# Optimization experiments

Measured on AMD Instinct MI355X. Metric: run time of the kernel, lower is better.

Reference implementation:

```python
import jax, jax.numpy as jnp
import numpy as np


def setup_inputs() -> dict:
    key = jax.random.key(0)
    ks = jax.random.split(key, 4)
    B, T, D, U = 256, 4096, 3, 8
    d = D + 1                      # time-augmented path dimension
    sig_dim = 1 + d + d * d        # depth-2 signature incl. constant term = 21
    glorot = jax.nn.initializers.glorot_uniform()
    return {
        "inputs": jax.random.normal(ks[0], (B, T, D), jnp.float32),
        "input_kernel": glorot(ks[1], (D, 3 * U), jnp.float32),
        "recurrent_kernel": glorot(ks[2], (U, 3 * U), jnp.float32),
        "forget_kernel": glorot(ks[3], (sig_dim, U), jnp.float32),
        "bias": jnp.zeros((4 * U,), jnp.float32),
    }


def _streamed_signature_depth2(path):
    """Streamed (cumulative) truncated signature of depth 2 via Chen's identity.
    path: (B, T, d) -> (B, T, 1 + d + d*d). Entry t is the signature of path[:t+1]."""
    B, T, d = path.shape
    dx = jnp.diff(path, axis=1)                                   # (B, T-1, d)
    L1 = jnp.cumsum(dx, axis=1)                                   # level-1
    L1_prev = jnp.concatenate([jnp.zeros((B, 1, d), path.dtype), L1[:, :-1]], axis=1)
    # Chen: L2_t = L2_{t-1} + L1_{t-1} (x) dx_t + 0.5 dx_t (x) dx_t
    terms = L1_prev[..., :, None] * dx[..., None, :] + 0.5 * dx[..., :, None] * dx[..., None, :]
    L2 = jnp.cumsum(terms, axis=1).reshape(B, T - 1, d * d)       # level-2
    sig = jnp.concatenate([jnp.ones((B, T - 1, 1), path.dtype), L1, L2], axis=-1)
    sig0 = jnp.concatenate(
        [jnp.ones((B, 1, 1), path.dtype), jnp.zeros((B, 1, d + d * d), path.dtype)], axis=-1)
    return jnp.concatenate([sig0, sig], axis=1)                   # (B, T, sig_dim)


def reference(inputs, input_kernel, recurrent_kernel, forget_kernel, bias):
    B, T, D = inputs.shape
    U = recurrent_kernel.shape[0]
    t_grid = jnp.linspace(0.0, 1.0, T)
    path = jnp.concatenate(
        [jnp.broadcast_to(t_grid[None, :, None], (B, T, 1)), inputs], axis=-1)
    sig = _streamed_signature_depth2(path)                        # (B, T, sig_dim)
    # normalize signatures at times t>0 by elapsed time (as in the original)
    sig = sig.at[:, 1:, :].set(sig[:, 1:, :] / t_grid[1:, None])

    b_i, b_f, b_c, b_o = jnp.split(bias, 4)
    x_proj = jnp.einsum('btd,du->btu', inputs, input_kernel)      # (B, T, 3U)

    def step(carry, xs):
        h, c = carry
        x_t, sig_t = xs
        gates = h @ recurrent_kernel + x_t                        # (B, 3U)
        i_t, c_hat, o_t = jnp.split(gates, 3, axis=-1)
        f_t = jax.nn.sigmoid(sig_t @ forget_kernel + b_f)         # signature forget gate
        i_t = jax.nn.sigmoid(i_t + b_i)
        c_hat = jnp.tanh(c_hat + b_c)
        o_t = jax.nn.sigmoid(o_t + b_o)
        c_new = f_t * c + i_t * c_hat
        h_new = o_t * jnp.tanh(c_new)
        return (h_new, c_new), h_new

    h0 = jnp.zeros((B, U), inputs.dtype)
    (_, _), h_seq = jax.lax.scan(
        step, (h0, h0), (x_proj.transpose(1, 0, 2), sig.transpose(1, 0, 2)))
    return h_seq.transpose(1, 0, 2)                               # (B, T, U)
```

## Files before the change

### kernel.cpp

```cpp
#include <hip/hip_runtime.h>
#include <hip/hip_bf16.h>

#define TT 4096
#define BB 256
#define DD 3
#define UU 8

#if defined(__has_builtin)
#if __has_builtin(__builtin_amdgcn_exp2f) && __has_builtin(__builtin_amdgcn_rcpf)
#define FAST_EXP2(x) __builtin_amdgcn_exp2f(x)
#define FAST_RCP(x)  __builtin_amdgcn_rcpf(x)
#endif
#endif
#ifndef FAST_EXP2
#define FAST_EXP2(x) exp2f(x)
#define FAST_RCP(x)  (1.0f / (x))
#endif

__device__ __forceinline__ float fsig(float x) {
    float e = FAST_EXP2(-1.4426950408889634f * x);
    return FAST_RCP(1.0f + e);
}
__device__ __forceinline__ float ftanh(float x) {
    float e = FAST_EXP2(2.8853900817779268f * x);
    return 1.0f - 2.0f * FAST_RCP(1.0f + e);
}

template <int CTRL>
__device__ __forceinline__ float dpp_f(float v) {
    int i = __builtin_bit_cast(int, v);
    i = __builtin_amdgcn_update_dpp(0, i, CTRL, 0xF, 0xF, true);
    return __builtin_bit_cast(float, i);
}

__device__ __forceinline__ float block_excl_scan(float v, int tid, float* red) {
    float x = v;
    int lid = tid & 63;
    #pragma unroll
    for (int d = 1; d < 64; d <<= 1) {
        float y = __shfl_up(x, d, 64);
        if (lid >= d) x += y;
    }
    int wave = tid >> 6;
    __syncthreads();
    if (lid == 63) red[wave] = x;
    __syncthreads();
    float off = 0.0f;
    for (int w = 0; w < wave; ++w) off += red[w];
    return off + (x - v);
}

__global__ __launch_bounds__(256) void sig_pre_kernel(
    const float* __restrict__ x,
    const float* __restrict__ Wi,
    const float* __restrict__ Wf,
    const float* __restrict__ bias,
    float* __restrict__ ws)
{
    __shared__ float sWf[21 * 8];
    __shared__ float sWi[3 * 24];
    __shared__ float sB[32];
    __shared__ float red[4];

    const int tid = threadIdx.x;
    const int b = blockIdx.x;
    if (tid < 168) sWf[tid] = Wf[tid];
    if (tid < 72)  sWi[tid] = Wi[tid];
    if (tid < 32)  sB[tid]  = bias[tid];
    __syncthreads();

    const float dtc = 1.0f / 4095.0f;
    const int t0 = tid * 16;
    const float* xb = x + (size_t)b * TT * DD;

    float l1[4] = {0.f, 0.f, 0.f, 0.f};
    float l2[16];
    #pragma unroll
    for (int i = 0; i < 16; ++i) l2[i] = 0.f;
    {
        int s = (tid == 0) ? 1 : t0;
        float xp0 = xb[(s - 1) * 3 + 0];
        float xp1 = xb[(s - 1) * 3 + 1];
        float xp2 = xb[(s - 1) * 3 + 2];
        for (; s < t0 + 16; ++s) {
            float c0 = xb[s * 3 + 0], c1 = xb[s * 3 + 1], c2 = xb[s * 3 + 2];
            float dxv[4] = {dtc, c0 - xp0, c1 - xp1, c2 - xp2};
            #pragma unroll
            for (int r = 0; r < 4; ++r) {
                float tr = l1[r] + 0.5f * dxv[r];
                #pragma unroll
                for (int cc = 0; cc < 4; ++cc)
                    l2[r * 4 + cc] = fmaf(tr, dxv[cc], l2[r * 4 + cc]);
            }
            #pragma unroll
            for (int r = 0; r < 4; ++r) l1[r] += dxv[r];
            xp0 = c0; xp1 = c1; xp2 = c2;
        }
    }

    float S1[4], O1[4];
    #pragma unroll
    for (int r = 0; r < 4; ++r) { S1[r] = l1[r]; }
    for (int r = 0; r < 4; ++r) O1[r] = block_excl_scan(S1[r], tid, red);
    float O2[16];
    for (int rc = 0; rc < 16; ++rc) {
        float c2v = l2[rc] + O1[rc >> 2] * S1[rc & 3];
        O2[rc] = block_excl_scan(c2v, tid, red);
    }

    #pragma unroll
    for (int r = 0; r < 4; ++r) l1[r] = O1[r];
    #pragma unroll
    for (int i = 0; i < 16; ++i) l2[i] = O2[i];

    float xp0, xp1, xp2;
    {
        int tp = (tid == 0) ? 0 : (t0 - 1);
        xp0 = xb[tp * 3 + 0]; xp1 = xb[tp * 3 + 1]; xp2 = xb[tp * 3 + 2];
    }
    for (int i2 = 0; i2 < 16; ++i2) {
        const int t = t0 + i2;
        float c0 = xb[t * 3 + 0], c1 = xb[t * 3 + 1], c2 = xb[t * 3 + 2];
        if (t > 0) {
            float dxv[4] = {dtc, c0 - xp0, c1 - xp1, c2 - xp2};
            #pragma unroll
            for (int r = 0; r < 4; ++r) {
                float tr = l1[r] + 0.5f * dxv[r];
                #pragma unroll
                for (int cc = 0; cc < 4; ++cc)
                    l2[r * 4 + cc] = fmaf(tr, dxv[cc], l2[r * 4 + cc]);
            }
            #pragma unroll
            for (int r = 0; r < 4; ++r) l1[r] += dxv[r];
        }
        xp0 = c0; xp1 = c1; xp2 = c2;
        const float scale = (t == 0) ? 1.0f : (4095.0f / (float)t);
        float sg[21];
        sg[0] = scale;
        #pragma unroll
        for (int r = 0; r < 4; ++r) sg[1 + r] = l1[r] * scale;
        #pragma unroll
        for (int rc = 0; rc < 16; ++rc) sg[5 + rc] = l2[rc] * scale;

        float fa[8];
        #pragma unroll
        for (int u = 0; u < 8; ++u) fa[u] = sB[8 + u];
        #pragma unroll
        for (int j = 0; j < 21; ++j) {
            float s = sg[j];
            #pragma unroll
            for (int u = 0; u < 8; ++u) fa[u] = fmaf(s, sWf[j * 8 + u], fa[u]);
        }
        float g[24];
        #pragma unroll
        for (int u = 0; u < 8; ++u) {
            g[u] = sB[u]; g[8 + u] = sB[16 + u]; g[16 + u] = sB[24 + u];
        }
        #pragma unroll
        for (int gg = 0; gg < 24; ++gg) {
            g[gg] = fmaf(c0, sWi[gg], g[gg]);
            g[gg] = fmaf(c1, sWi[24 + gg], g[gg]);
            g[gg] = fmaf(c2, sWi[48 + gg], g[gg]);
        }
        float4* wp = (float4*)ws + ((size_t)t * BB + b) * UU;
        #pragma unroll
        for (int u = 0; u < 8; ++u)
            wp[u] = make_float4(g[u], g[8 + u], g[16 + u], fsig(fa[u]));
    }
}

__global__ __launch_bounds__(64) void lstm_scan_full(
    const float* __restrict__ ws, const float* __restrict__ Wr,
    float* __restrict__ out)
{
    const int lane = threadIdx.x;
    const int u = lane & 7;
    const int b = blockIdx.x * 8 + (lane >> 3);
    float wa[8], wb[8], wc[8];
    #pragma unroll
    for (int m = 0; m < 8; ++m) {
        int j = u ^ m;
        wa[m] = Wr[j * 24 + u];
        wb[m] = Wr[j * 24 + 8 + u];
        wc[m] = Wr[j * 24 + 16 + u];
    }
    const float4* gp = (const float4*)ws + (size_t)b * 8 + u;
    float4 buf[8];
    #pragma unroll
    for (int p = 0; p < 8; ++p) buf[p] = gp[(size_t)p * 2048];
    float h = 0.f, c = 0.f;
    float* op = out + (size_t)b * TT * 8 + u;

    auto step = [&](int t, float4 g) {
        float h1 = dpp_f<0xB1>(h);
        float h2 = dpp_f<0x4E>(h);
        float h3 = dpp_f<0x1B>(h);
        float h7 = dpp_f<0x141>(h);
        float h6 = dpp_f<0xB1>(h7);
        float h5 = dpp_f<0x4E>(h7);
        float h4 = dpp_f<0x1B>(h7);
        float gi = fmaf(h, wa[0], g.x), giB = h4 * wa[4];
        float gc = fmaf(h, wb[0], g.y), gcB = h4 * wb[4];
        float go = fmaf(h, wc[0], g.z), goB = h4 * wc[4];
        gi = fmaf(h1, wa[1], gi);  giB = fmaf(h5, wa[5], giB);
        gc = fmaf(h1, wb[1], gc);  gcB = fmaf(h5, wb[5], gcB);
        go = fmaf(h1, wc[1], go);  goB = fmaf(h5, wc[5], goB);
        gi = fmaf(h2, wa[2], gi);  giB = fmaf(h6, wa[6], giB);
        gc = fmaf(h2, wb[2], gc);  gcB = fmaf(h6, wb[6], gcB);
        go = fmaf(h2, wc[2], go);  goB = fmaf(h6, wc[6], goB);
        gi = fmaf(h3, wa[3], gi);  giB = fmaf(h7, wa[7], giB);
        gc = fmaf(h3, wb[3], gc);  gcB = fmaf(h7, wb[7], gcB);
        go = fmaf(h3, wc[3], go);  goB = fmaf(h7, wc[7], goB);
        gi += giB; gc += gcB; go += goB;
        float iv = fsig(gi);
        float cv = ftanh(gc);
        float ov = fsig(go);
        c = fmaf(g.w, c, iv * cv);
        h = ov * ftanh(c);
        op[(size_t)t * 8] = h;
    };

    for (int tb = 0; tb + 8 < TT; tb += 8) {
        #pragma unroll
        for (int j = 0; j < 8; ++j) {
            const int t = tb + j;
            float4 g = buf[j];
            buf[j] = gp[(size_t)(t + 8) * 2048];
            step(t, g);
        }
    }
    #pragma unroll
    for (int j = 0; j < 8; ++j) step(TT - 8 + j, buf[j]);
}

__global__ __launch_bounds__(64) void lstm_scan_ultra(
    const float* __restrict__ x, const float* __restrict__ Wi,
    const float* __restrict__ Wr, const float* __restrict__ Wf,
    const float* __restrict__ bias, float* __restrict__ out)
{
    const int lane = threadIdx.x;
    const int u = lane & 7;
    const int q = lane >> 3;
    const int b = blockIdx.x * 8 + q;
    float wa[8], wb[8], wc[8];
    #pragma unroll
    for (int m = 0; m < 8; ++m) {
        int j = u ^ m;
        wa[m] = Wr[j * 24 + u];
        wb[m] = Wr[j * 24 + 8 + u];
        wc[m] = Wr[j * 24 + 16 + u];
    }
    float wia[3], wib[3], wic[3];
    #pragma unroll
    for (int k = 0; k < 3; ++k) {
        wia[k] = Wi[k * 24 + u];
        wib[k] = Wi[k * 24 + 8 + u];
        wic[k] = Wi[k * 24 + 16 + u];
    }
    float wf[21];
    #pragma unroll
    for (int j = 0; j < 21; ++j) wf[j] = Wf[j * 8 + u];
    const float bi = bias[u], bf = bias[8 + u], bc = bias[16 + u], bo = bias[24 + u];
    const float* xb = x + (size_t)b * TT * 3;
    float l1[4] = {0.f, 0.f, 0.f, 0.f};
    float l2[16];
    #pragma unroll
    for (int i = 0; i < 16; ++i) l2[i] = 0.f;
    float xp0 = xb[0], xp1 = xb[1], xp2 = xb[2];
    float h = 0.f, c = 0.f;
    float* op = out + (size_t)b * TT * 8 + u;
    const float dtc = 1.0f / 4095.0f;
    for (int t = 0; t < TT; ++t) {
        float c0 = xb[t * 3 + 0], c1 = xb[t * 3 + 1], c2 = xb[t * 3 + 2];
        if (t > 0) {
            float dxv[4] = {dtc, c0 - xp0, c1 - xp1, c2 - xp2};
            #pragma unroll
            for (int r = 0; r < 4; ++r) {
                float tr = l1[r] + 0.5f * dxv[r];
                #pragma unroll
                for (int cc = 0; cc < 4; ++cc)
                    l2[r * 4 + cc] = fmaf(tr, dxv[cc], l2[r * 4 + cc]);
            }
            #pragma unroll
            for (int r = 0; r < 4; ++r) l1[r] += dxv[r];
        }
        xp0 = c0; xp1 = c1; xp2 = c2;
        const float scale = (t == 0) ? 1.0f : (4095.0f / (float)t);
        float dot = wf[0];
        #pragma unroll
        for (int r = 0; r < 4; ++r) dot = fmaf(l1[r], wf[1 + r], dot);
        #pragma unroll
        for (int rc = 0; rc < 16; ++rc) dot = fmaf(l2[rc], wf[5 + rc], dot);
        float fv = fsig(fmaf(scale, dot, bf));
        float gi = bi, gc = bc, go = bo;
        gi = fmaf(c0, wia[0], gi); gi = fmaf(c1, wia[1], gi); gi = fmaf(c2, wia[2], gi);
        gc = fmaf(c0, wib[0], gc); gc = fmaf(c1, wib[1], gc); gc = fmaf(c2, wib[2], gc);
        go = fmaf(c0, wic[0], go); go = fmaf(c1, wic[1], go); go = fmaf(c2, wic[2], go);
        float h1 = dpp_f<0xB1>(h);
        float h2 = dpp_f<0x4E>(h);
        float h3 = dpp_f<0x1B>(h);
        float h7 = dpp_f<0x141>(h);
        float h6 = dpp_f<0xB1>(h7);
        float h5 = dpp_f<0x4E>(h7);
        float h4 = dpp_f<0x1B>(h7);
        gi = fmaf(h, wa[0], gi); gi = fmaf(h1, wa[1], gi); gi = fmaf(h2, wa[2], gi); gi = fmaf(h3, wa[3], gi);
        gi = fmaf(h4, wa[4], gi); gi = fmaf(h5, wa[5], gi); gi = fmaf(h6, wa[6], gi); gi = fmaf(h7, wa[7], gi);
        gc = fmaf(h, wb[0], gc); gc = fmaf(h1, wb[1], gc); gc = fmaf(h2, wb[2], gc); gc = fmaf(h3, wb[3], gc);
        gc = fmaf(h4, wb[4], gc); gc = fmaf(h5, wb[5], gc); gc = fmaf(h6, wb[6], gc); gc = fmaf(h7, wb[7], gc);
        go = fmaf(h, wc[0], go); go = fmaf(h1, wc[1], go); go = fmaf(h2, wc[2], go); go = fmaf(h3, wc[3], go);
        go = fmaf(h4, wc[4], go); go = fmaf(h5, wc[5], go); go = fmaf(h6, wc[6], go); go = fmaf(h7, wc[7], go);
        float iv = fsig(gi);
        float cv = ftanh(gc);
        float ov = fsig(go);
        c = fmaf(fv, c, iv * cv);
        h = ov * ftanh(c);
        op[(size_t)t * 8] = h;
    }
}

extern "C" void kernel_launch(void* const* d_in, const int* in_sizes, int n_in,
                              void* d_out, int out_size, void* d_ws, size_t ws_size,
                              hipStream_t stream) {
    const float* x    = (const float*)d_in[0];
    const float* Wi   = (const float*)d_in[1];
    const float* Wr   = (const float*)d_in[2];
    const float* Wf   = (const float*)d_in[3];
    const float* bias = (const float*)d_in[4];
    float* out = (float*)d_out;

    const size_t need = (size_t)TT * BB * UU * 4 * sizeof(float);
    if (ws_size >= need) {
        sig_pre_kernel<<<dim3(BB), dim3(256), 0, stream>>>(x, Wi, Wf, bias, (float*)d_ws);
        lstm_scan_full<<<dim3(BB / 8), dim3(64), 0, stream>>>((const float*)d_ws, Wr, out);
    } else {
        lstm_scan_ultra<<<dim3(BB / 8), dim3(64), 0, stream>>>(x, Wi, Wr, Wf, bias, out);
    }
}
```

Measured before the change: 652.5 us.

## Fold log2e scaling into weights, merge gate reciprocals, use DPP wave scans

Pre-scales the input, recurrent, forget weights and biases by -log2e or 2log2e so the activation exponents need no extra multiply. In the recurrent step, each pair of sigmoid/tanh reciprocals is combined into a single reciprocal of a product, which shortens the per-step serial dependency chain. The signature precompute now loads its inputs as vectorised registers, replaces the shuffle-based block scans with DPP wave scans plus one shared-memory pass, and applies the time normalisation once after the forget-gate dot product. The trade-off is slightly different rounding behaviour and a clamp needed to avoid overflow in the merged expressions.

```diff
diff --git a/kernel.cpp b/kernel.cpp
--- a/kernel.cpp
+++ b/kernel.cpp
@@ -17,13 +17,12 @@
 #define FAST_RCP(x)  (1.0f / (x))
 #endif
 
+#define NLOG2E  (-1.4426950408889634f)
+#define P2LOG2E ( 2.8853900817779268f)
+
 __device__ __forceinline__ float fsig(float x) {
-    float e = FAST_EXP2(-1.4426950408889634f * x);
+    float e = FAST_EXP2(NLOG2E * x);
     return FAST_RCP(1.0f + e);
-}
-__device__ __forceinline__ float ftanh(float x) {
-    float e = FAST_EXP2(2.8853900817779268f * x);
-    return 1.0f - 2.0f * FAST_RCP(1.0f + e);
 }
 
 template <int CTRL>
@@ -32,22 +31,19 @@
     i = __builtin_amdgcn_update_dpp(0, i, CTRL, 0xF, 0xF, true);
     return __builtin_bit_cast(float, i);
 }
-
-__device__ __forceinline__ float block_excl_scan(float v, int tid, float* red) {
-    float x = v;
-    int lid = tid & 63;
-    #pragma unroll
-    for (int d = 1; d < 64; d <<= 1) {
-        float y = __shfl_up(x, d, 64);
-        if (lid >= d) x += y;
-    }
-    int wave = tid >> 6;
-    __syncthreads();
-    if (lid == 63) red[wave] = x;
-    __syncthreads();
-    float off = 0.0f;
-    for (int w = 0; w < wave; ++w) off += red[w];
-    return off + (x - v);
+template <int CTRL, int RM>
+__device__ __forceinline__ float dpp_add(float x) {
+    int t = __builtin_amdgcn_update_dpp(0, __builtin_bit_cast(int, x), CTRL, RM, 0xF, true);
+    return x + __builtin_bit_cast(float, t);
+}
+__device__ __forceinline__ float wave_incl_scan(float v) {
+    v = dpp_add<0x111, 0xF>(v);
+    v = dpp_add<0x112, 0xF>(v);
+    v = dpp_add<0x114, 0xF>(v);
+    v = dpp_add<0x118, 0xF>(v);
+    v = dpp_add<0x142, 0xA>(v);
+    v = dpp_add<0x143, 0xC>(v);
+    return v;
 }
 
 __global__ __launch_bounds__(256) void sig_pre_kernel(
@@ -57,34 +53,57 @@
     const float* __restrict__ bias,
     float* __restrict__ ws)
 {
-    __shared__ float sWf[21 * 8];
-    __shared__ float sWi[3 * 24];
+    __shared__ float sWf[168];
+    __shared__ float sWi[72];
     __shared__ float sB[32];
-    __shared__ float red[4];
+    __shared__ float tot1[4 * 4];
+    __shared__ float tot2[4 * 16];
 
     const int tid = threadIdx.x;
     const int b = blockIdx.x;
-    if (tid < 168) sWf[tid] = Wf[tid];
-    if (tid < 72)  sWi[tid] = Wi[tid];
-    if (tid < 32)  sB[tid]  = bias[tid];
+    if (tid < 168) sWf[tid] = NLOG2E * Wf[tid];
+    if (tid < 72) {
+        int col = tid % 24;
+        float s = (col < 8) ? NLOG2E : (col < 16) ? P2LOG2E : NLOG2E;
+        sWi[tid] = s * Wi[tid];
+    }
+    if (tid < 32) {
+        float s = (tid < 16) ? NLOG2E : (tid < 24) ? P2LOG2E : NLOG2E;
+        sB[tid] = s * bias[tid];
+    }
     __syncthreads();
 
     const float dtc = 1.0f / 4095.0f;
     const int t0 = tid * 16;
+    const int lid = tid & 63;
+    const int wv = tid >> 6;
     const float* xb = x + (size_t)b * TT * DD;
+
+    float xs[48];
+    {
+        const float4* xv = (const float4*)(xb + (size_t)t0 * 3);
+        #pragma unroll
+        for (int k = 0; k < 12; ++k) {
+            float4 v = xv[k];
+            xs[k * 4 + 0] = v.x; xs[k * 4 + 1] = v.y;
+            xs[k * 4 + 2] = v.z; xs[k * 4 + 3] = v.w;
+        }
+    }
+    float pp0, pp1, pp2;
+    if (tid == 0) { pp0 = xs[0]; pp1 = xs[1]; pp2 = xs[2]; }
+    else { pp0 = xb[t0 * 3 - 3]; pp1 = xb[t0 * 3 - 2]; pp2 = xb[t0 * 3 - 1]; }
 
     float l1[4] = {0.f, 0.f, 0.f, 0.f};
     float l2[16];
     #pragma unroll
     for (int i = 0; i < 16; ++i) l2[i] = 0.f;
     {
-        int s = (tid == 0) ? 1 : t0;
-        float xp0 = xb[(s - 1) * 3 + 0];
-        float xp1 = xb[(s - 1) * 3 + 1];
-        float xp2 = xb[(s - 1) * 3 + 2];
-        for (; s < t0 + 16; ++s) {
-            float c0 = xb[s * 3 + 0], c1 = xb[s * 3 + 1], c2 = xb[s * 3 + 2];
-            float dxv[4] = {dtc, c0 - xp0, c1 - xp1, c2 - xp2};
+        float xp0 = pp0, xp1 = pp1, xp2 = pp2;
+        #pragma unroll
+        for (int i = 0; i < 16; ++i) {
+            float c0 = xs[i * 3], c1 = xs[i * 3 + 1], c2 = xs[i * 3 + 2];
+            float d0 = (tid == 0 && i == 0) ? 0.f : dtc;
+            float dxv[4] = {d0, c0 - xp0, c1 - xp1, c2 - xp2};
             #pragma unroll
             for (int r = 0; r < 4; ++r) {
                 float tr = l1[r] + 0.5f * dxv[r];
@@ -98,14 +117,34 @@
         }
     }
 
-    float S1[4], O1[4];
-    #pragma unroll
-    for (int r = 0; r < 4; ++r) { S1[r] = l1[r]; }
-    for (int r = 0; r < 4; ++r) O1[r] = block_excl_scan(S1[r], tid, red);
-    float O2[16];
+    float I1[4], O1[4];
+    #pragma unroll
+    for (int r = 0; r < 4; ++r) {
+        I1[r] = wave_incl_scan(l1[r]);
+        if (lid == 63) tot1[wv * 4 + r] = I1[r];
+    }
+    __syncthreads();
+    #pragma unroll
+    for (int r = 0; r < 4; ++r) {
+        float off = 0.f;
+        for (int w = 0; w < wv; ++w) off += tot1[w * 4 + r];
+        O1[r] = off + I1[r] - l1[r];
+    }
+
+    float I2[16], cin[16], O2[16];
+    #pragma unroll
     for (int rc = 0; rc < 16; ++rc) {
-        float c2v = l2[rc] + O1[rc >> 2] * S1[rc & 3];
-        O2[rc] = block_excl_scan(c2v, tid, red);
+        float c2v = l2[rc] + O1[rc >> 2] * l1[rc & 3];
+        cin[rc] = c2v;
+        I2[rc] = wave_incl_scan(c2v);
+        if (lid == 63) tot2[wv * 16 + rc] = I2[rc];
+    }
+    __syncthreads();
+    #pragma unroll
+    for (int rc = 0; rc < 16; ++rc) {
+        float off = 0.f;
+        for (int w = 0; w < wv; ++w) off += tot2[w * 16 + rc];
+        O2[rc] = off + I2[rc] - cin[rc];
     }
 
     #pragma unroll
@@ -113,43 +152,39 @@
     #pragma unroll
     for (int i = 0; i < 16; ++i) l2[i] = O2[i];
 
-    float xp0, xp1, xp2;
-    {
-        int tp = (tid == 0) ? 0 : (t0 - 1);
-        xp0 = xb[tp * 3 + 0]; xp1 = xb[tp * 3 + 1]; xp2 = xb[tp * 3 + 2];
-    }
+    float xp0 = pp0, xp1 = pp1, xp2 = pp2;
+    #pragma unroll
     for (int i2 = 0; i2 < 16; ++i2) {
         const int t = t0 + i2;
-        float c0 = xb[t * 3 + 0], c1 = xb[t * 3 + 1], c2 = xb[t * 3 + 2];
-        if (t > 0) {
-            float dxv[4] = {dtc, c0 - xp0, c1 - xp1, c2 - xp2};
-            #pragma unroll
-            for (int r = 0; r < 4; ++r) {
-                float tr = l1[r] + 0.5f * dxv[r];
-                #pragma unroll
-                for (int cc = 0; cc < 4; ++cc)
-                    l2[r * 4 + cc] = fmaf(tr, dxv[cc], l2[r * 4 + cc]);
-            }
-            #pragma unroll
-            for (int r = 0; r < 4; ++r) l1[r] += dxv[r];
-        }
+        float c0 = xs[i2 * 3], c1 = xs[i2 * 3 + 1], c2 = xs[i2 * 3 + 2];
+        float d0 = (tid == 0 && i2 == 0) ? 0.f : dtc;
+        float dxv[4] = {d0, c0 - xp0, c1 - xp1, c2 - xp2};
+        #pragma unroll
+        for (int r = 0; r < 4; ++r) {
+            float tr = l1[r] + 0.5f * dxv[r];
+            #pragma unroll
+            for (int cc = 0; cc < 4; ++cc)
+                l2[r * 4 + cc] = fmaf(tr, dxv[cc], l2[r * 4 + cc]);
+        }
+        #pragma unroll
+        for (int r = 0; r < 4; ++r) l1[r] += dxv[r];
         xp0 = c0; xp1 = c1; xp2 = c2;
+
         const float scale = (t == 0) ? 1.0f : (4095.0f / (float)t);
-        float sg[21];
-        sg[0] = scale;
-        #pragma unroll
-        for (int r = 0; r < 4; ++r) sg[1 + r] = l1[r] * scale;
-        #pragma unroll
-        for (int rc = 0; rc < 16; ++rc) sg[5 + rc] = l2[rc] * scale;
-
         float fa[8];
         #pragma unroll
-        for (int u = 0; u < 8; ++u) fa[u] = sB[8 + u];
-        #pragma unroll
-        for (int j = 0; j < 21; ++j) {
-            float s = sg[j];
-            #pragma unroll
-            for (int u = 0; u < 8; ++u) fa[u] = fmaf(s, sWf[j * 8 + u], fa[u]);
+        for (int u = 0; u < 8; ++u) fa[u] = sWf[u];
+        #pragma unroll
+        for (int r = 0; r < 4; ++r) {
+            float s = l1[r];
+            #pragma unroll
+            for (int u = 0; u < 8; ++u) fa[u] = fmaf(s, sWf[(1 + r) * 8 + u], fa[u]);
+        }
+        #pragma unroll
+        for (int rc = 0; rc < 16; ++rc) {
+            float s = l2[rc];
+            #pragma unroll
+            for (int u = 0; u < 8; ++u) fa[u] = fmaf(s, sWf[(5 + rc) * 8 + u], fa[u]);
         }
         float g[24];
         #pragma unroll
@@ -164,8 +199,11 @@
         }
         float4* wp = (float4*)ws + ((size_t)t * BB + b) * UU;
         #pragma unroll
-        for (int u = 0; u < 8; ++u)
-            wp[u] = make_float4(g[u], g[8 + u], g[16 + u], fsig(fa[u]));
+        for (int u = 0; u < 8; ++u) {
+            float fav = fmaf(scale, fa[u], sB[8 + u]);
+            float f = FAST_RCP(1.0f + FAST_EXP2(fav));
+            wp[u] = make_float4(g[u], g[8 + u], g[16 + u], f);
+        }
     }
 }
 
@@ -180,9 +218,9 @@
     #pragma unroll
     for (int m = 0; m < 8; ++m) {
         int j = u ^ m;
-        wa[m] = Wr[j * 24 + u];
-        wb[m] = Wr[j * 24 + 8 + u];
-        wc[m] = Wr[j * 24 + 16 + u];
+        wa[m] = NLOG2E  * Wr[j * 24 + u];
+        wb[m] = P2LOG2E * Wr[j * 24 + 8 + u];
+        wc[m] = NLOG2E  * Wr[j * 24 + 16 + u];
     }
     const float4* gp = (const float4*)ws + (size_t)b * 8 + u;
     float4 buf[8];
@@ -212,11 +250,15 @@
         gc = fmaf(h3, wb[3], gc);  gcB = fmaf(h7, wb[7], gcB);
         go = fmaf(h3, wc[3], go);  goB = fmaf(h7, wc[7], goB);
         gi += giB; gc += gcB; go += goB;
-        float iv = fsig(gi);
-        float cv = ftanh(gc);
-        float ov = fsig(go);
-        c = fmaf(g.w, c, iv * cv);
-        h = ov * ftanh(c);
+        float ei = FAST_EXP2(gi);
+        float ec = FAST_EXP2(gc);
+        float eo = FAST_EXP2(go);
+        float r1 = FAST_RCP((1.0f + ei) * (1.0f + ec));
+        c = fmaf(g.w, c, (ec - 1.0f) * r1);
+        float s3 = fminf(P2LOG2E * c, 63.0f);
+        float e2c = FAST_EXP2(s3);
+        float r2 = FAST_RCP((1.0f + eo) * (1.0f + e2c));
+        h = (e2c - 1.0f) * r2;
         op[(size_t)t * 8] = h;
     };
 
@@ -310,10 +352,11 @@
         go = fmaf(h, wc[0], go); go = fmaf(h1, wc[1], go); go = fmaf(h2, wc[2], go); go = fmaf(h3, wc[3], go);
         go = fmaf(h4, wc[4], go); go = fmaf(h5, wc[5], go); go = fmaf(h6, wc[6], go); go = fmaf(h7, wc[7], go);
         float iv = fsig(gi);
-        float cv = ftanh(gc);
+        float cv = 1.0f - 2.0f * FAST_RCP(1.0f + FAST_EXP2(P2LOG2E * gc));
         float ov = fsig(go);
         c = fmaf(fv, c, iv * cv);
-        h = ov * ftanh(c);
+        float s3 = fminf(P2LOG2E * c, 63.0f);
+        h = ov * (1.0f - 2.0f * FAST_RCP(1.0f + FAST_EXP2(s3)));
         op[(size_t)t * 8] = h;
     }
 }
```

After: 784.7 us. 1.2x slower.

## Interleave four independent batch chains per wave and fold exp constants into weights

Applied to the files above, without the earlier changes.

The scan kernel now gives each wave four batch groups (32 batches instead of 8), so four independent recurrences are interleaved to hide the latency of the serial DPP/FMA/transcendental chain. The log2e scaling factors are folded into the precomputed gate inputs and the recurrent weights, and the sigmoid*tanh products are merged so each pair shares one reciprocal. Together these shorten the per-step dependency chain. In exchange only 8 blocks are launched, using far fewer CUs, and register pressure rises with the four prefetch buffers.

```diff
diff --git a/kernel.cpp b/kernel.cpp
--- a/kernel.cpp
+++ b/kernel.cpp
@@ -17,12 +17,15 @@
 #define FAST_RCP(x)  (1.0f / (x))
 #endif
 
+#define NLOG2E  (-1.4426950408889634f)
+#define P2LOG2E ( 2.8853900817779268f)
+
 __device__ __forceinline__ float fsig(float x) {
-    float e = FAST_EXP2(-1.4426950408889634f * x);
+    float e = FAST_EXP2(NLOG2E * x);
     return FAST_RCP(1.0f + e);
 }
 __device__ __forceinline__ float ftanh(float x) {
-    float e = FAST_EXP2(2.8853900817779268f * x);
+    float e = FAST_EXP2(P2LOG2E * x);
     return 1.0f - 2.0f * FAST_RCP(1.0f + e);
 }
 
@@ -165,7 +168,8 @@
         float4* wp = (float4*)ws + ((size_t)t * BB + b) * UU;
         #pragma unroll
         for (int u = 0; u < 8; ++u)
-            wp[u] = make_float4(g[u], g[8 + u], g[16 + u], fsig(fa[u]));
+            wp[u] = make_float4(NLOG2E * g[u], P2LOG2E * g[8 + u],
+                                NLOG2E * g[16 + u], fsig(fa[u]));
     }
 }
 
@@ -175,62 +179,101 @@
 {
     const int lane = threadIdx.x;
     const int u = lane & 7;
-    const int b = blockIdx.x * 8 + (lane >> 3);
+    const int q = lane >> 3;
+    const int b0 = blockIdx.x * 32 + q;
     float wa[8], wb[8], wc[8];
     #pragma unroll
     for (int m = 0; m < 8; ++m) {
         int j = u ^ m;
-        wa[m] = Wr[j * 24 + u];
-        wb[m] = Wr[j * 24 + 8 + u];
-        wc[m] = Wr[j * 24 + 16 + u];
-    }
-    const float4* gp = (const float4*)ws + (size_t)b * 8 + u;
-    float4 buf[8];
-    #pragma unroll
-    for (int p = 0; p < 8; ++p) buf[p] = gp[(size_t)p * 2048];
-    float h = 0.f, c = 0.f;
-    float* op = out + (size_t)b * TT * 8 + u;
-
-    auto step = [&](int t, float4 g) {
-        float h1 = dpp_f<0xB1>(h);
-        float h2 = dpp_f<0x4E>(h);
-        float h3 = dpp_f<0x1B>(h);
-        float h7 = dpp_f<0x141>(h);
-        float h6 = dpp_f<0xB1>(h7);
-        float h5 = dpp_f<0x4E>(h7);
-        float h4 = dpp_f<0x1B>(h7);
-        float gi = fmaf(h, wa[0], g.x), giB = h4 * wa[4];
-        float gc = fmaf(h, wb[0], g.y), gcB = h4 * wb[4];
-        float go = fmaf(h, wc[0], g.z), goB = h4 * wc[4];
-        gi = fmaf(h1, wa[1], gi);  giB = fmaf(h5, wa[5], giB);
-        gc = fmaf(h1, wb[1], gc);  gcB = fmaf(h5, wb[5], gcB);
-        go = fmaf(h1, wc[1], go);  goB = fmaf(h5, wc[5], goB);
-        gi = fmaf(h2, wa[2], gi);  giB = fmaf(h6, wa[6], giB);
-        gc = fmaf(h2, wb[2], gc);  gcB = fmaf(h6, wb[6], gcB);
-        go = fmaf(h2, wc[2], go);  goB = fmaf(h6, wc[6], goB);
-        gi = fmaf(h3, wa[3], gi);  giB = fmaf(h7, wa[7], giB);
-        gc = fmaf(h3, wb[3], gc);  gcB = fmaf(h7, wb[7], gcB);
-        go = fmaf(h3, wc[3], go);  goB = fmaf(h7, wc[7], goB);
-        gi += giB; gc += gcB; go += goB;
-        float iv = fsig(gi);
-        float cv = ftanh(gc);
-        float ov = fsig(go);
-        c = fmaf(g.w, c, iv * cv);
-        h = ov * ftanh(c);
-        op[(size_t)t * 8] = h;
+        wa[m] = NLOG2E  * Wr[j * 24 + u];
+        wb[m] = P2LOG2E * Wr[j * 24 + 8 + u];
+        wc[m] = NLOG2E  * Wr[j * 24 + 16 + u];
+    }
+    const float4* gp[4];
+    float* op[4];
+    float h[4], c[4];
+    float4 buf[4][8];
+    #pragma unroll
+    for (int n = 0; n < 4; ++n) {
+        int b = b0 + n * 8;
+        gp[n] = (const float4*)ws + (size_t)b * 8 + u;
+        op[n] = out + (size_t)b * TT * 8 + u;
+        h[n] = 0.f; c[n] = 0.f;
+        #pragma unroll
+        for (int p = 0; p < 8; ++p) buf[n][p] = gp[n][(size_t)p * 2048];
+    }
+
+    auto round = [&](int t, int j, bool pf) {
+        float gx[4], gy[4], gz[4], gw[4];
+        #pragma unroll
+        for (int n = 0; n < 4; ++n) {
+            float4 g = buf[n][j];
+            gx[n] = g.x; gy[n] = g.y; gz[n] = g.z; gw[n] = g.w;
+        }
+        if (pf) {
+            #pragma unroll
+            for (int n = 0; n < 4; ++n)
+                buf[n][j] = gp[n][(size_t)(t + 8) * 2048];
+        }
+        float H[4][8];
+        #pragma unroll
+        for (int n = 0; n < 4; ++n) {
+            H[n][0] = h[n];
+            H[n][1] = dpp_f<0xB1>(h[n]);
+            H[n][2] = dpp_f<0x4E>(h[n]);
+            H[n][3] = dpp_f<0x1B>(h[n]);
+            H[n][7] = dpp_f<0x141>(h[n]);
+            H[n][6] = dpp_f<0xB1>(H[n][7]);
+            H[n][5] = dpp_f<0x4E>(H[n][7]);
+            H[n][4] = dpp_f<0x1B>(H[n][7]);
+        }
+        float gi[4], gcv[4], go[4];
+        #pragma unroll
+        for (int n = 0; n < 4; ++n) {
+            float a0 = fmaf(H[n][0], wa[0], gx[n]), a1 = H[n][4] * wa[4];
+            float b0_ = fmaf(H[n][0], wb[0], gy[n]), b1 = H[n][4] * wb[4];
+            float c0_ = fmaf(H[n][0], wc[0], gz[n]), c1 = H[n][4] * wc[4];
+            a0 = fmaf(H[n][1], wa[1], a0);  a1 = fmaf(H[n][5], wa[5], a1);
+            b0_ = fmaf(H[n][1], wb[1], b0_); b1 = fmaf(H[n][5], wb[5], b1);
+            c0_ = fmaf(H[n][1], wc[1], c0_); c1 = fmaf(H[n][5], wc[5], c1);
+            a0 = fmaf(H[n][2], wa[2], a0);  a1 = fmaf(H[n][6], wa[6], a1);
+            b0_ = fmaf(H[n][2], wb[2], b0_); b1 = fmaf(H[n][6], wb[6], b1);
+            c0_ = fmaf(H[n][2], wc[2], c0_); c1 = fmaf(H[n][6], wc[6], c1);
+            a0 = fmaf(H[n][3], wa[3], a0);  a1 = fmaf(H[n][7], wa[7], a1);
+            b0_ = fmaf(H[n][3], wb[3], b0_); b1 = fmaf(H[n][7], wb[7], b1);
+            c0_ = fmaf(H[n][3], wc[3], c0_); c1 = fmaf(H[n][7], wc[7], c1);
+            gi[n] = a0 + a1; gcv[n] = b0_ + b1; go[n] = c0_ + c1;
+        }
+        float ei[4], ec[4], eo[4];
+        #pragma unroll
+        for (int n = 0; n < 4; ++n) {
+            ei[n] = FAST_EXP2(gi[n]);
+            ec[n] = FAST_EXP2(gcv[n]);
+            eo[n] = FAST_EXP2(go[n]);
+        }
+        #pragma unroll
+        for (int n = 0; n < 4; ++n) {
+            float r1 = FAST_RCP((1.0f + ei[n]) * (1.0f + ec[n]));
+            c[n] = fmaf(gw[n], c[n], (ec[n] - 1.0f) * r1);
+        }
+        #pragma unroll
+        for (int n = 0; n < 4; ++n) {
+            float s3 = fminf(P2LOG2E * c[n], 63.0f);
+            float e2 = FAST_EXP2(s3);
+            float r2 = FAST_RCP((1.0f + eo[n]) * (1.0f + e2));
+            h[n] = (e2 - 1.0f) * r2;
+        }
+        #pragma unroll
+        for (int n = 0; n < 4; ++n)
+            op[n][(size_t)t * 8] = h[n];
     };
 
-    for (int tb = 0; tb + 8 < TT; tb += 8) {
-        #pragma unroll
-        for (int j = 0; j < 8; ++j) {
-            const int t = tb + j;
-            float4 g = buf[j];
-            buf[j] = gp[(size_t)(t + 8) * 2048];
-            step(t, g);
-        }
-    }
-    #pragma unroll
-    for (int j = 0; j < 8; ++j) step(TT - 8 + j, buf[j]);
+    for (int tb = 0; tb + 8 <= TT - 8; tb += 8) {
+        #pragma unroll
+        for (int j = 0; j < 8; ++j) round(tb + j, j, true);
+    }
+    #pragma unroll
+    for (int j = 0; j < 8; ++j) round(TT - 8 + j, j, false);
 }
 
 __global__ __launch_bounds__(64) void lstm_scan_ultra(
@@ -331,7 +374,7 @@
     const size_t need = (size_t)TT * BB * UU * 4 * sizeof(float);
     if (ws_size >= need) {
         sig_pre_kernel<<<dim3(BB), dim3(256), 0, stream>>>(x, Wi, Wf, bias, (float*)d_ws);
-        lstm_scan_full<<<dim3(BB / 8), dim3(64), 0, stream>>>((const float*)d_ws, Wr, out);
+        lstm_scan_full<<<dim3(BB / 32), dim3(64), 0, stream>>>((const float*)d_ws, Wr, out);
     } else {
         lstm_scan_ultra<<<dim3(BB / 8), dim3(64), 0, stream>>>(x, Wi, Wr, Wf, bias, out);
     }
```

Result: slower. 1.899 ms (+191.0%).

## Interleave two batch chains per lane and fold exp2 scaling into weights

Applied to the files above, without the earlier changes.

The scan kernel now handles two independent batch recurrences per lane, so the dependent DPP/FMA/transcendental chains of one can overlap with the other's. It launches half as many blocks. The log2e factors are folded into the precomputed gates and recurrent weights, which removes a multiply before each exp2. Prefetch depth drops from 8 to 4 steps per chain. Occupancy falls to 16 waves, so total parallelism is lower, but each wave gets more instruction-level parallelism on the latency-bound serial chain.

```diff
diff --git a/kernel.cpp b/kernel.cpp
--- a/kernel.cpp
+++ b/kernel.cpp
@@ -17,12 +17,15 @@
 #define FAST_RCP(x)  (1.0f / (x))
 #endif
 
+#define NLOG2E  (-1.4426950408889634f)
+#define P2LOG2E ( 2.8853900817779268f)
+
 __device__ __forceinline__ float fsig(float x) {
-    float e = FAST_EXP2(-1.4426950408889634f * x);
+    float e = FAST_EXP2(NLOG2E * x);
     return FAST_RCP(1.0f + e);
 }
 __device__ __forceinline__ float ftanh(float x) {
-    float e = FAST_EXP2(2.8853900817779268f * x);
+    float e = FAST_EXP2(P2LOG2E * x);
     return 1.0f - 2.0f * FAST_RCP(1.0f + e);
 }
 
@@ -165,7 +168,8 @@
         float4* wp = (float4*)ws + ((size_t)t * BB + b) * UU;
         #pragma unroll
         for (int u = 0; u < 8; ++u)
-            wp[u] = make_float4(g[u], g[8 + u], g[16 + u], fsig(fa[u]));
+            wp[u] = make_float4(NLOG2E * g[u], P2LOG2E * g[8 + u],
+                                NLOG2E * g[16 + u], fsig(fa[u]));
     }
 }
 
@@ -175,62 +179,89 @@
 {
     const int lane = threadIdx.x;
     const int u = lane & 7;
-    const int b = blockIdx.x * 8 + (lane >> 3);
+    const int q = lane >> 3;
+    const int b0 = blockIdx.x * 16 + q;
     float wa[8], wb[8], wc[8];
     #pragma unroll
     for (int m = 0; m < 8; ++m) {
         int j = u ^ m;
-        wa[m] = Wr[j * 24 + u];
-        wb[m] = Wr[j * 24 + 8 + u];
-        wc[m] = Wr[j * 24 + 16 + u];
-    }
-    const float4* gp = (const float4*)ws + (size_t)b * 8 + u;
-    float4 buf[8];
-    #pragma unroll
-    for (int p = 0; p < 8; ++p) buf[p] = gp[(size_t)p * 2048];
-    float h = 0.f, c = 0.f;
-    float* op = out + (size_t)b * TT * 8 + u;
-
-    auto step = [&](int t, float4 g) {
-        float h1 = dpp_f<0xB1>(h);
-        float h2 = dpp_f<0x4E>(h);
-        float h3 = dpp_f<0x1B>(h);
-        float h7 = dpp_f<0x141>(h);
-        float h6 = dpp_f<0xB1>(h7);
-        float h5 = dpp_f<0x4E>(h7);
-        float h4 = dpp_f<0x1B>(h7);
-        float gi = fmaf(h, wa[0], g.x), giB = h4 * wa[4];
-        float gc = fmaf(h, wb[0], g.y), gcB = h4 * wb[4];
-        float go = fmaf(h, wc[0], g.z), goB = h4 * wc[4];
-        gi = fmaf(h1, wa[1], gi);  giB = fmaf(h5, wa[5], giB);
-        gc = fmaf(h1, wb[1], gc);  gcB = fmaf(h5, wb[5], gcB);
-        go = fmaf(h1, wc[1], go);  goB = fmaf(h5, wc[5], goB);
-        gi = fmaf(h2, wa[2], gi);  giB = fmaf(h6, wa[6], giB);
-        gc = fmaf(h2, wb[2], gc);  gcB = fmaf(h6, wb[6], gcB);
-        go = fmaf(h2, wc[2], go);  goB = fmaf(h6, wc[6], goB);
-        gi = fmaf(h3, wa[3], gi);  giB = fmaf(h7, wa[7], giB);
-        gc = fmaf(h3, wb[3], gc);  gcB = fmaf(h7, wb[7], gcB);
-        go = fmaf(h3, wc[3], go);  goB = fmaf(h7, wc[7], goB);
-        gi += giB; gc += gcB; go += goB;
-        float iv = fsig(gi);
-        float cv = ftanh(gc);
-        float ov = fsig(go);
-        c = fmaf(g.w, c, iv * cv);
-        h = ov * ftanh(c);
-        op[(size_t)t * 8] = h;
+        wa[m] = NLOG2E  * Wr[j * 24 + u];
+        wb[m] = P2LOG2E * Wr[j * 24 + 8 + u];
+        wc[m] = NLOG2E  * Wr[j * 24 + 16 + u];
+    }
+    const float4* gp0 = (const float4*)ws + (size_t)b0 * 8 + u;
+    const float4* gp1 = gp0 + 64;
+    float* op0 = out + (size_t)b0 * TT * 8 + u;
+    float* op1 = op0 + (size_t)8 * TT * 8;
+    float4 bufA[4], bufB[4];
+    #pragma unroll
+    for (int p = 0; p < 4; ++p) {
+        bufA[p] = gp0[(size_t)p * 2048];
+        bufB[p] = gp1[(size_t)p * 2048];
+    }
+    float h0 = 0.f, c0 = 0.f, h1 = 0.f, c1 = 0.f;
+
+    auto step2 = [&](int t, int j, bool pf) {
+        float4 ga = bufA[j];
+        float4 gb = bufB[j];
+        if (pf) {
+            bufA[j] = gp0[(size_t)(t + 4) * 2048];
+            bufB[j] = gp1[(size_t)(t + 4) * 2048];
+        }
+        float A0 = h0, A1 = dpp_f<0xB1>(h0), A2 = dpp_f<0x4E>(h0), A3 = dpp_f<0x1B>(h0);
+        float A7 = dpp_f<0x141>(h0), A6 = dpp_f<0xB1>(A7), A5 = dpp_f<0x4E>(A7), A4 = dpp_f<0x1B>(A7);
+        float B0 = h1, B1 = dpp_f<0xB1>(h1), B2 = dpp_f<0x4E>(h1), B3 = dpp_f<0x1B>(h1);
+        float B7 = dpp_f<0x141>(h1), B6 = dpp_f<0xB1>(B7), B5 = dpp_f<0x4E>(B7), B4 = dpp_f<0x1B>(B7);
+        float giA = fmaf(A0, wa[0], ga.x), giA2 = A4 * wa[4];
+        float gcA = fmaf(A0, wb[0], ga.y), gcA2 = A4 * wb[4];
+        float goA = fmaf(A0, wc[0], ga.z), goA2 = A4 * wc[4];
+        float giB = fmaf(B0, wa[0], gb.x), giB2 = B4 * wa[4];
+        float gcB = fmaf(B0, wb[0], gb.y), gcB2 = B4 * wb[4];
+        float goB = fmaf(B0, wc[0], gb.z), goB2 = B4 * wc[4];
+        giA = fmaf(A1, wa[1], giA); giA2 = fmaf(A5, wa[5], giA2);
+        gcA = fmaf(A1, wb[1], gcA); gcA2 = fmaf(A5, wb[5], gcA2);
+        goA = fmaf(A1, wc[1], goA); goA2 = fmaf(A5, wc[5], goA2);
+        giB = fmaf(B1, wa[1], giB); giB2 = fmaf(B5, wa[5], giB2);
+        gcB = fmaf(B1, wb[1], gcB); gcB2 = fmaf(B5, wb[5], gcB2);
+        goB = fmaf(B1, wc[1], goB); goB2 = fmaf(B5, wc[5], goB2);
+        giA = fmaf(A2, wa[2], giA); giA2 = fmaf(A6, wa[6], giA2);
+        gcA = fmaf(A2, wb[2], gcA); gcA2 = fmaf(A6, wb[6], gcA2);
+        goA = fmaf(A2, wc[2], goA); goA2 = fmaf(A6, wc[6], goA2);
+        giB = fmaf(B2, wa[2], giB); giB2 = fmaf(B6, wa[6], giB2);
+        gcB = fmaf(B2, wb[2], gcB); gcB2 = fmaf(B6, wb[6], gcB2);
+        goB = fmaf(B2, wc[2], goB); goB2 = fmaf(B6, wc[6], goB2);
+        giA = fmaf(A3, wa[3], giA); giA2 = fmaf(A7, wa[7], giA2);
+        gcA = fmaf(A3, wb[3], gcA); gcA2 = fmaf(A7, wb[7], gcA2);
+        goA = fmaf(A3, wc[3], goA); goA2 = fmaf(A7, wc[7], goA2);
+        giB = fmaf(B3, wa[3], giB); giB2 = fmaf(B7, wa[7], giB2);
+        gcB = fmaf(B3, wb[3], gcB); gcB2 = fmaf(B7, wb[7], gcB2);
+        goB = fmaf(B3, wc[3], goB); goB2 = fmaf(B7, wc[7], goB2);
+        giA += giA2; gcA += gcA2; goA += goA2;
+        giB += giB2; gcB += gcB2; goB += goB2;
+        float eiA = FAST_EXP2(giA), ecA = FAST_EXP2(gcA), eoA = FAST_EXP2(goA);
+        float eiB = FAST_EXP2(giB), ecB = FAST_EXP2(gcB), eoB = FAST_EXP2(goB);
+        float ivA = FAST_RCP(1.0f + eiA);
+        float cvA = fmaf(-2.0f, FAST_RCP(1.0f + ecA), 1.0f);
+        float ovA = FAST_RCP(1.0f + eoA);
+        float ivB = FAST_RCP(1.0f + eiB);
+        float cvB = fmaf(-2.0f, FAST_RCP(1.0f + ecB), 1.0f);
+        float ovB = FAST_RCP(1.0f + eoB);
+        c0 = fmaf(ga.w, c0, ivA * cvA);
+        c1 = fmaf(gb.w, c1, ivB * cvB);
+        float e2A = FAST_EXP2(P2LOG2E * c0);
+        float e2B = FAST_EXP2(P2LOG2E * c1);
+        h0 = ovA * fmaf(-2.0f, FAST_RCP(1.0f + e2A), 1.0f);
+        h1 = ovB * fmaf(-2.0f, FAST_RCP(1.0f + e2B), 1.0f);
+        op0[(size_t)t * 8] = h0;
+        op1[(size_t)t * 8] = h1;
     };
 
-    for (int tb = 0; tb + 8 < TT; tb += 8) {
-        #pragma unroll
-        for (int j = 0; j < 8; ++j) {
-            const int t = tb + j;
-            float4 g = buf[j];
-            buf[j] = gp[(size_t)(t + 8) * 2048];
-            step(t, g);
-        }
-    }
-    #pragma unroll
-    for (int j = 0; j < 8; ++j) step(TT - 8 + j, buf[j]);
+    for (int tb = 0; tb < TT - 4; tb += 4) {
+        #pragma unroll
+        for (int j = 0; j < 4; ++j) step2(tb + j, j, true);
+    }
+    #pragma unroll
+    for (int j = 0; j < 4; ++j) step2(TT - 4 + j, j, false);
 }
 
 __global__ __launch_bounds__(64) void lstm_scan_ultra(
@@ -331,7 +362,7 @@
     const size_t need = (size_t)TT * BB * UU * 4 * sizeof(float);
     if (ws_size >= need) {
         sig_pre_kernel<<<dim3(BB), dim3(256), 0, stream>>>(x, Wi, Wf, bias, (float*)d_ws);
-        lstm_scan_full<<<dim3(BB / 8), dim3(64), 0, stream>>>((const float*)d_ws, Wr, out);
+        lstm_scan_full<<<dim3(BB / 16), dim3(64), 0, stream>>>((const float*)d_ws, Wr, out);
     } else {
         lstm_scan_ultra<<<dim3(BB / 8), dim3(64), 0, stream>>>(x, Wi, Wr, Wf, bias, out);
     }
```

Measured after the change: 1.049 ms. 60.7% more time.
